# Kernel optimization log

Hardware: AMD Instinct MI355X
Metric: run time of the kernel (lower is better)

Reference implementation:

```python
import jax, jax.numpy as jnp
import numpy as np
import math

B, L, HID, H = 16, 1024, 1024, 16
E = HID // H
HALF = L // 2 + 1                      # 513 rfft bins
GLOBAL_RATIO = 0.6
LEFT = int(HALF * (1.0 - GLOBAL_RATIO))  # 205 (i=0, filter_mixer='G')
RIGHT = HALF                            # 513
FACTOR = 1
TOP_K = int(FACTOR * math.log(L))       # 6
LN_EPS = 1e-12


def setup_inputs() -> dict:
    key = jax.random.key(0)
    ks = jax.random.split(key, 12)
    s = 0.02
    return {
        "input_tensor": jax.random.normal(ks[0], (B, L, HID), jnp.float32),
        "attention_mask": jnp.zeros((B, 1, 1, L), jnp.float32),
        "Wq": jax.random.normal(ks[1], (HID, HID), jnp.float32) * s,
        "bq": jnp.zeros((HID,), jnp.float32),
        "Wk": jax.random.normal(ks[2], (HID, HID), jnp.float32) * s,
        "bk": jnp.zeros((HID,), jnp.float32),
        "Wv": jax.random.normal(ks[3], (HID, HID), jnp.float32) * s,
        "bv": jnp.zeros((HID,), jnp.float32),
        "Wd": jax.random.normal(ks[4], (HID, HID), jnp.float32) * s,
        "bd": jnp.zeros((HID,), jnp.float32),
        "gamma": jnp.ones((HID,), jnp.float32),
        "beta": jnp.zeros((HID,), jnp.float32),
    }


def _heads(x):  # [B,L,HID] -> [B,H,E,L]
    return x.reshape(B, L, H, E).transpose(0, 2, 3, 1)


def _layer_norm(x, gamma, beta):
    mu = jnp.mean(x, axis=-1, keepdims=True)
    var = jnp.var(x, axis=-1, keepdims=True)
    return (x - mu) / jnp.sqrt(var + LN_EPS) * gamma + beta


def reference(input_tensor, attention_mask, Wq, bq, Wk, bk, Wv, bv, Wd, bd, gamma, beta):
    # QKV projections -> [B,H,E,L]
    q = _heads(input_tensor @ Wq + bq)
    k = _heads(input_tensor @ Wk + bk)
    v = _heads(input_tensor @ Wv + bv)

    # FFT-based autocorrelation restricted to retained frequency band [LEFT,RIGHT)
    q_fft = jnp.fft.rfft(q, axis=-1)            # [B,H,E,HALF] complex64
    k_fft = jnp.fft.rfft(k, axis=-1)
    res = q_fft[..., LEFT:RIGHT] * jnp.conj(k_fft[..., LEFT:RIGHT])
    box = jnp.zeros((B, H, E, HALF), res.dtype).at[..., LEFT:RIGHT].set(res)
    corr = jnp.fft.irfft(box, n=L, axis=-1)     # [B,H,E,L]

    # time_delay_agg_training: topk shared delays, softmax-weighted roll aggregation
    mean_value = jnp.mean(corr, axis=(1, 2))            # [B,L]
    _, idx = jax.lax.top_k(jnp.mean(mean_value, axis=0), TOP_K)  # [TOP_K]
    weights = mean_value[:, idx]                         # [B,TOP_K]
    tmp_corr = jax.nn.softmax(weights, axis=-1)
    delays_agg = jnp.zeros_like(v)
    for i in range(TOP_K):  # TOP_K=6, fixed small loop
        pattern = jnp.roll(v, -idx[i], axis=-1)
        delays_agg = delays_agg + pattern * tmp_corr[:, i][:, None, None, None]

    # [B,H,E,L] -> [B,L,HID]
    context = delays_agg.transpose(0, 3, 1, 2).reshape(B, L, HID)
    hidden = context @ Wd + bd
    return _layer_norm(hidden + input_tensor, gamma, beta)
```

## Files before the change

kernel.cpp:

```cpp
#include <hip/hip_runtime.h>


typedef unsigned short u16;
typedef unsigned int   u32;
typedef __attribute__((ext_vector_type(8))) __bf16 bf16x8;
typedef __attribute__((ext_vector_type(4))) float  floatx4;

#define HIDn 1024

__device__ __forceinline__ u16 f2b(float f){ u32 i = __float_as_uint(f); return (u16)((i + 0x7fffu + ((i>>16)&1u)) >> 16); }

__device__ __forceinline__ void gl_lds16(const u16* g, u16* l){
  __builtin_amdgcn_global_load_lds((__attribute__((address_space(1))) const void*)g,
                                   (__attribute__((address_space(3))) void*)l, 16, 0, 0);
}

__device__ __forceinline__ void bar(){
  asm volatile("" ::: "memory");
  __builtin_amdgcn_s_barrier();
  asm volatile("" ::: "memory");
}
__device__ __forceinline__ void lgkm0(){
  asm volatile("s_waitcnt lgkmcnt(0)" ::: "memory");
  __builtin_amdgcn_sched_barrier(0);
}

__global__ void fill_kernel(float* __restrict__ out, float v, int n)
{
  const int i = blockIdx.x*blockDim.x + threadIdx.x;
  if (i < n) out[i] = v;
}

__global__ __launch_bounds__(1024)
void prep_kernel(const float* __restrict__ x, u16* __restrict__ xb,
                 float* __restrict__ cbuf, int* __restrict__ ctrs,
                 const float* __restrict__ Wq, const float* __restrict__ Wk,
                 const float* __restrict__ Wv, const float* __restrict__ Wd,
                 u16* __restrict__ WqkvT, u16* __restrict__ WdT)
{
  __shared__ float tile[32][33];
  if (blockIdx.x < 2048){
    const int i = blockIdx.x*1024 + threadIdx.x;
    if (i < 16384) cbuf[i] = 0.f;
    if (blockIdx.x == 0 && threadIdx.x < 8) ctrs[threadIdx.x] = 0;
    const float4* xp = (const float4*)x;
    const float4 a = xp[2*i], b = xp[2*i+1];
    uint4 o;
    o.x = (u32)f2b(a.x) | ((u32)f2b(a.y)<<16);
    o.y = (u32)f2b(a.z) | ((u32)f2b(a.w)<<16);
    o.z = (u32)f2b(b.x) | ((u32)f2b(b.y)<<16);
    o.w = (u32)f2b(b.z) | ((u32)f2b(b.w)<<16);
    ((uint4*)xb)[i] = o;
  } else {
    const int bb  = blockIdx.x - 2048;
    const int mat = bb >> 10;
    const int rem = bb & 1023;
    const int bxT = rem & 31, byT = rem >> 5;
    const int tx = threadIdx.x & 31, ty = threadIdx.x >> 5;
    const float* W = (mat==0)?Wq:(mat==1)?Wk:(mat==2)?Wv:Wd;
    const int k = byT*32 + ty, n = bxT*32 + tx;
    tile[ty][tx] = W[(long)k*HIDn + n];
    __syncthreads();
    const int on = bxT*32 + ty, ok = byT*32 + tx;
    const u16 val = f2b(tile[tx][ty]);
    if (mat < 3) WqkvT[(long)(mat*HIDn + on)*HIDn + ok] = val;
    else         WdT[(long)on*HIDn + ok] = val;
  }
}

template<int EPI>
__global__ __launch_bounds__(512, 2)
void gemm_mfma(const u16* __restrict__ A, int lda, long sA,
               const u16* __restrict__ Bt, int ldb, long sB,
               void* __restrict__ C0, u16* __restrict__ o1, u16* __restrict__ o2,
               int ldc, int K,
               const float* __restrict__ b0, const float* __restrict__ b1,
               const float* __restrict__ b2, const float* __restrict__ resid,
               float* __restrict__ cbuf, int* __restrict__ ctrs,
               const float* __restrict__ gam, const float* __restrict__ bet,
               int* __restrict__ idxo, float* __restrict__ wo)
{
  __shared__ __align__(16) u16 As[2][16384];
  __shared__ __align__(16) u16 Bs[2][16384];
  __shared__ float bins[512];
  __shared__ int lastf;

  const int gx = gridDim.x, gy = gridDim.y;
  const int lin = (blockIdx.z*gy + blockIdx.y)*gx + blockIdx.x;
  const int cpx = (gx*gy*gridDim.z) >> 3;
  const int swz = (lin & 7)*cpx + (lin >> 3);
  const int bx  = swz % gx;
  const int byz = swz / gx;
  const int by  = byz % gy;
  const int bz  = byz / gy;

  const int tid  = threadIdx.x;
  const int wave = tid >> 6, lane = tid & 63;
  const int waveM = wave >> 2, waveN = wave & 3;
  const int qd = lane >> 4, ln = lane & 15, rl = ln & 7;
  const u16* Ab = A  + (long)bz * sA;
  const u16* Bb = Bt + (long)bz * sB;
  const int aRow0 = by * 256, bRow0 = bx * 256;
  const int nt = K >> 6;

  const int s0 = wave*128 + lane;
  const int r0 = s0 >> 3, r1 = r0 + 8;
  const int kc = ((s0 & 7) ^ (r0 & 7)) * 8;
  const long aOff0 = (long)(aRow0 + r0)*lda + kc;
  const long aOff1 = (long)(aRow0 + r1)*lda + kc;
  const long bOff0 = (long)(bRow0 + r0)*ldb + kc;
  const long bOff1 = (long)(bRow0 + r1)*ldb + kc;
  const int dstW = wave*1024;

#define STAGE_A(p, h, kt) do{ \
    gl_lds16(Ab + aOff0 + (long)(h)*128*lda + (kt), &As[p][(h)*8192 + dstW]); \
    gl_lds16(Ab + aOff1 + (long)(h)*128*lda + (kt), &As[p][(h)*8192 + dstW + 512]); }while(0)
#define STAGE_B(p, h, kt) do{ \
    gl_lds16(Bb + bOff0 + (long)(h)*128*ldb + (kt), &Bs[p][(h)*8192 + dstW]); \
    gl_lds16(Bb + bOff1 + (long)(h)*128*ldb + (kt), &Bs[p][(h)*8192 + dstW + 512]); }while(0)

  if (EPI == 3) bins[tid] = 0.f;

  floatx4 acc[8][4];
  const floatx4 z4 = {0.f, 0.f, 0.f, 0.f};
  #pragma unroll
  for (int i=0;i<8;++i)
    #pragma unroll
    for (int j=0;j<4;++j) acc[i][j] = z4;

  const int aRd = (waveM*128 + ln)*64;
  const int bRd = (waveN*64  + ln)*64;
  const int csw0 = ((0 + qd) ^ rl) * 8;
  const int csw1 = ((4 + qd) ^ rl) * 8;

  bf16x8 av0[4], av1[4];
  bf16x8 bvA0[2], bvA1[2];
  bf16x8 bvB0[2], bvB1[2];

#define DS_AV(BUF, MH) do{ const u16* Ap_ = &As[BUF][0]; \
    _Pragma("unroll") for (int mi=0;mi<4;++mi){ \
      av0[mi] = *(const bf16x8*)(Ap_ + aRd + (MH)*4096 + mi*1024 + csw0); \
      av1[mi] = *(const bf16x8*)(Ap_ + aRd + (MH)*4096 + mi*1024 + csw1); } }while(0)
#define DS_BV(BUF, NH, d0_, d1_) do{ const u16* Bp_ = &Bs[BUF][0]; \
    _Pragma("unroll") for (int ni=0;ni<2;++ni){ \
      d0_[ni] = *(const bf16x8*)(Bp_ + bRd + ((NH)*2+ni)*1024 + csw0); \
      d1_[ni] = *(const bf16x8*)(Bp_ + bRd + ((NH)*2+ni)*1024 + csw1); } }while(0)
#define MFMAQ(MH, NH, b0_, b1_) do{ \
    __builtin_amdgcn_sched_barrier(0); \
    __builtin_amdgcn_s_setprio(1); \
    _Pragma("unroll") for (int mi=0;mi<4;++mi) \
      _Pragma("unroll") for (int ni=0;ni<2;++ni){ \
        acc[(MH)*4+mi][(NH)*2+ni] = __builtin_amdgcn_mfma_f32_16x16x32_bf16(av0[mi], b0_[ni], acc[(MH)*4+mi][(NH)*2+ni],0,0,0); \
        acc[(MH)*4+mi][(NH)*2+ni] = __builtin_amdgcn_mfma_f32_16x16x32_bf16(av1[mi], b1_[ni], acc[(MH)*4+mi][(NH)*2+ni],0,0,0); } \
    __builtin_amdgcn_s_setprio(0); \
    __builtin_amdgcn_sched_barrier(0); }while(0)

  STAGE_B(0,0,0);  STAGE_B(0,1,0);  STAGE_A(0,0,0);  STAGE_A(0,1,0);
  STAGE_B(1,0,64); STAGE_B(1,1,64); STAGE_A(1,0,64); STAGE_A(1,1,64);
  asm volatile("s_waitcnt vmcnt(8)" ::: "memory");
  bar();

  const int nIt = nt >> 1;
  for (int it = 0; it < nIt-1; ++it){
    const int k2 = (it*2+2) << 6;
    const int k3 = (it*2+3) << 6;
    DS_AV(0,0); DS_BV(0,0,bvA0,bvA1);
    bar(); lgkm0(); MFMAQ(0,0,bvA0,bvA1); bar();
    DS_BV(0,1,bvB0,bvB1);
    bar(); lgkm0(); MFMAQ(0,1,bvB0,bvB1); bar();
    DS_AV(0,1); STAGE_B(0,0,k2);
    bar(); lgkm0(); MFMAQ(1,0,bvA0,bvA1); bar();
    STAGE_B(0,1,k2);
    asm volatile("s_waitcnt vmcnt(4)" ::: "memory");
    bar(); MFMAQ(1,1,bvB0,bvB1); bar();
    DS_AV(1,0); DS_BV(1,0,bvA0,bvA1); STAGE_A(0,0,k2);
    bar(); lgkm0(); MFMAQ(0,0,bvA0,bvA1); bar();
    DS_BV(1,1,bvB0,bvB1); STAGE_A(0,1,k2);
    bar(); lgkm0(); MFMAQ(0,1,bvB0,bvB1); bar();
    DS_AV(1,1); STAGE_B(1,0,k3);
    bar(); lgkm0(); MFMAQ(1,0,bvA0,bvA1); bar();
    STAGE_B(1,1,k3); STAGE_A(1,0,k3); STAGE_A(1,1,k3);
    asm volatile("s_waitcnt vmcnt(8)" ::: "memory");
    bar(); MFMAQ(1,1,bvB0,bvB1); bar();
  }
  DS_AV(0,0); DS_BV(0,0,bvA0,bvA1);
  bar(); lgkm0(); MFMAQ(0,0,bvA0,bvA1); bar();
  DS_BV(0,1,bvB0,bvB1);
  bar(); lgkm0(); MFMAQ(0,1,bvB0,bvB1); bar();
  DS_AV(0,1);
  bar(); lgkm0(); MFMAQ(1,0,bvA0,bvA1); bar();
  asm volatile("s_waitcnt vmcnt(0)" ::: "memory");
  bar(); MFMAQ(1,1,bvB0,bvB1); bar();
  DS_AV(1,0); DS_BV(1,0,bvA0,bvA1);
  bar(); lgkm0(); MFMAQ(0,0,bvA0,bvA1); bar();
  DS_BV(1,1,bvB0,bvB1);
  bar(); lgkm0(); MFMAQ(0,1,bvB0,bvB1); bar();
  DS_AV(1,1);
  bar(); lgkm0(); MFMAQ(1,0,bvA0,bvA1); bar();
  MFMAQ(1,1,bvB0,bvB1);
#undef STAGE_A
#undef STAGE_B
#undef DS_AV
#undef DS_BV
#undef MFMAQ

  if (EPI == 3){
    float dsum[11][4];
    #pragma unroll
    for (int dd=0; dd<11; ++dd)
      #pragma unroll
      for (int r=0;r<4;++r) dsum[dd][r] = 0.f;
    #pragma unroll
    for (int mi=0;mi<8;++mi)
      #pragma unroll
      for (int ni=0;ni<4;++ni){
        const int dd = mi - ni + 3;
        #pragma unroll
        for (int r=0;r<4;++r) dsum[dd][r] += acc[mi][ni][r];
      }
    const int base = 255 + 128*waveM - 64*waveN + 4*qd - ln;
    #pragma unroll
    for (int dd=0; dd<11; ++dd)
      #pragma unroll
      for (int r=0;r<4;++r)
        atomicAdd(&bins[base + 16*(dd-3) + r], dsum[dd][r]);
    __syncthreads();
    if (tid < 511){
      const int d = (aRow0 - bRow0 + tid - 255) & 1023;
      atomicAdd(cbuf + bz*1024 + d, bins[tid]);
    }
    __syncthreads();
    if (tid == 0){
      __threadfence();
      const int nb = gx*gy*gridDim.z;
      lastf = (atomicAdd(ctrs, 1) == nb-1);
    }
    __syncthreads();
    if (!lastf) return;
    __threadfence();
    float* csh  = (float*)&As[0][0];
    float* gshp = (float*)&Bs[0][0];
    float* csum = gshp + 1024;
    float* vals = csum + 1024;
    float* wvp  = vals + 1024;
    int*   wip  = (int*)(wvp + 16);
    int*   chos = wip + 16;
    float* pw   = (float*)(chos + 8);
    for (int i = tid; i < 16384; i += 512) csh[i] = cbuf[i];
    __syncthreads();
    for (int l = tid; l < 1024; l += 512){
      float sc = 0.f;
      #pragma unroll
      for (int b = 0; b < 16; ++b) sc += csh[b*1024 + l];
      csum[l] = sc;
      float s;
      if (l == 0) s = 307.f;
      else {
        const float kk = 3.14159265358979e0f/1024.f;
        const int n1 = (307*l) & 2047, n2 = (716*l) & 2047;
        s = sinf((float)n1*kk) * cosf((float)n2*kk) / sinf((float)l*kk);
      }
      gshp[l] = (2.f*s + ((l & 1) ? -1.f : 1.f)) * (1.0f/1048576.0f);
    }
    __syncthreads();
    for (int l = tid; l < 1024; l += 512){
      float S = 0.f;
      #pragma unroll 4
      for (int m = 0; m < 1024; ++m) S += csum[m] * gshp[(l - m) & 1023];
      vals[l] = S;
    }
    __syncthreads();
    for (int r = 0; r < 6; ++r){
      float v1 = vals[tid], v2 = vals[tid + 512];
      float cv = v1; int ci = tid;
      if (v2 > v1){ cv = v2; ci = tid + 512; }
      #pragma unroll
      for (int off = 32; off > 0; off >>= 1){
        const float ov = __shfl_down(cv, off);
        const int   oi = __shfl_down(ci, off);
        if (ov > cv || (ov == cv && oi < ci)){ cv = ov; ci = oi; }
      }
      if (lane == 0){ wvp[wave] = cv; wip[wave] = ci; }
      __syncthreads();
      if (tid == 0){
        float bv = wvp[0]; int bi = wip[0];
        #pragma unroll
        for (int k2 = 1; k2 < 8; ++k2)
          if (wvp[k2] > bv || (wvp[k2] == bv && wip[k2] < bi)){ bv = wvp[k2]; bi = wip[k2]; }
        chos[r] = bi; idxo[r] = bi; vals[bi] = -3.0e38f;
      }
      __syncthreads();
    }
    if (tid < 384){
      const int p = tid >> 2, li = tid & 3;
      const int b = p / 6, i = p % 6, ch = chos[i];
      float a2 = 0.f;
      #pragma unroll 4
      for (int m = li*256; m < li*256 + 256; ++m) a2 += csh[b*1024 + m] * gshp[(ch - m) & 1023];
      a2 += __shfl_down(a2, 2);
      a2 += __shfl_down(a2, 1);
      if (li == 0) pw[p] = a2;
    }
    __syncthreads();
    if (tid < 16){
      float w[6]; float mx = -3.0e38f;
      #pragma unroll
      for (int i = 0; i < 6; ++i){ w[i] = pw[tid*6 + i]; mx = fmaxf(mx, w[i]); }
      float sum = 0.f;
      #pragma unroll
      for (int i = 0; i < 6; ++i){ w[i] = expf(w[i] - mx); sum += w[i]; }
      #pragma unroll
      for (int i = 0; i < 6; ++i) wo[tid*6 + i] = w[i] / sum;
    }
    return;
  }

  if (EPI == 0){
    const int which = bx >> 2;
    const float* bp = (which==0) ? b0 : ((which==1) ? b1 : b2);
    u16* Cb = (which==0) ? (u16*)C0 : ((which==1) ? o1 : o2);
    const int nb = bRow0 & 1023;
    #pragma unroll
    for (int mi=0;mi<8;++mi){
      const int gm = aRow0 + waveM*128 + mi*16 + qd*4;
      #pragma unroll
      for (int ni=0;ni<4;++ni){
        const int nl = nb + waveN*64 + ni*16 + ln;
        const float bias = bp[nl];
        #pragma unroll
        for (int r=0;r<4;++r) Cb[(long)(gm+r)*ldc + nl] = f2b(acc[mi][ni][r] + bias);
      }
    }
  } else {
    float* C = (float*)C0;
    #pragma unroll
    for (int mi=0;mi<8;++mi){
      const int gm = aRow0 + waveM*128 + mi*16 + qd*4;
      #pragma unroll
      for (int ni=0;ni<4;++ni){
        const int gn = bRow0 + waveN*64 + ni*16 + ln;
        const float bias = b0[gn];
        #pragma unroll
        for (int r=0;r<4;++r)
          C[(long)(gm+r)*ldc + gn] = acc[mi][ni][r] + bias + resid[(long)(gm+r)*ldc + gn];
      }
    }
    const int nb = gx*gy*gridDim.z;
    __syncthreads();
    if (tid == 0){
      __threadfence();
      atomicAdd(&ctrs[1], 1);
      while (atomicAdd(&ctrs[1], 0) < nb) __builtin_amdgcn_s_sleep(8);
    }
    __syncthreads();
    __threadfence();
    float* gsh_ = (float*)&As[0][0];
    float* bsh_ = gsh_ + 1024;
    for (int i = tid; i < 1024; i += 512){ gsh_[i] = gam[i]; bsh_[i] = bet[i]; }
    __syncthreads();
    const float4* g4 = (const float4*)gsh_;
    const float4* be4 = (const float4*)bsh_;
    const int row0 = lin*64 + wave*8;
    for (int rr = 0; rr < 8; ++rr){
      const int row = row0 + rr;
      float4* rp = (float4*)(C + (long)row*1024);
      float4 vv[4]; float s1 = 0.f, s2 = 0.f;
      #pragma unroll
      for (int j = 0; j < 4; ++j){
        vv[j] = rp[j*64 + lane];
        s1 += vv[j].x + vv[j].y + vv[j].z + vv[j].w;
        s2 += vv[j].x*vv[j].x + vv[j].y*vv[j].y + vv[j].z*vv[j].z + vv[j].w*vv[j].w;
      }
      #pragma unroll
      for (int off = 32; off > 0; off >>= 1){
        s1 += __shfl_xor(s1, off);
        s2 += __shfl_xor(s2, off);
      }
      const float mu   = s1 * (1.f/1024.f);
      const float var  = fmaxf(s2 * (1.f/1024.f) - mu*mu, 0.f);
      const float rstd = rsqrtf(var + 1e-12f);
      #pragma unroll
      for (int j = 0; j < 4; ++j){
        const int idx = j*64 + lane;
        const float4 g = g4[idx], be = be4[idx];
        float4 o;
        o.x = (vv[j].x - mu)*rstd*g.x + be.x;
        o.y = (vv[j].y - mu)*rstd*g.y + be.y;
        o.z = (vv[j].z - mu)*rstd*g.z + be.z;
        o.w = (vv[j].w - mu)*rstd*g.w + be.w;
        rp[idx] = o;
      }
    }
  }
}

__global__ __launch_bounds__(256)
void context_kernel(const u16* __restrict__ Vb, const int* __restrict__ idx,
                    const float* __restrict__ w, u16* __restrict__ CT)
{
  const int lin = blockIdx.x;
  const int xcd = lin & 7, j = lin >> 3;
  const int row = xcd*2048 + j*2 + (threadIdx.x >> 7);
  const int b = row >> 10, l = row & 1023;
  const int t = threadIdx.x & 127;
  float wl[6]; int id[6];
  #pragma unroll
  for (int i = 0; i < 6; ++i){ id[i] = idx[i]; wl[i] = w[b*6 + i]; }
  float acc[8] = {0,0,0,0,0,0,0,0};
  #pragma unroll
  for (int i = 0; i < 6; ++i){
    const long src = (long)b*1024 + ((l + id[i]) & 1023);
    const uint4 pk = *(const uint4*)(Vb + src*1024 + t*8);
    const float ww = wl[i];
    union{float f; u32 u;} cv;
    cv.u = pk.x<<16;          acc[0] += ww*cv.f;
    cv.u = pk.x & 0xffff0000u; acc[1] += ww*cv.f;
    cv.u = pk.y<<16;          acc[2] += ww*cv.f;
    cv.u = pk.y & 0xffff0000u; acc[3] += ww*cv.f;
    cv.u = pk.z<<16;          acc[4] += ww*cv.f;
    cv.u = pk.z & 0xffff0000u; acc[5] += ww*cv.f;
    cv.u = pk.w<<16;          acc[6] += ww*cv.f;
    cv.u = pk.w & 0xffff0000u; acc[7] += ww*cv.f;
  }
  uint4 o;
  o.x = (u32)f2b(acc[0]) | ((u32)f2b(acc[1])<<16);
  o.y = (u32)f2b(acc[2]) | ((u32)f2b(acc[3])<<16);
  o.z = (u32)f2b(acc[4]) | ((u32)f2b(acc[5])<<16);
  o.w = (u32)f2b(acc[6]) | ((u32)f2b(acc[7])<<16);
  *(uint4*)(CT + (long)row*1024 + t*8) = o;
}

extern "C" void kernel_launch(void* const* d_in, const int* in_sizes, int n_in,
                              void* d_out, int out_size, void* d_ws, size_t ws_size,
                              hipStream_t stream)
{
  (void)in_sizes; (void)n_in;
  const float* x     = (const float*)d_in[0];
  const float* Wq    = (const float*)d_in[2];
  const float* bq    = (const float*)d_in[3];
  const float* Wk    = (const float*)d_in[4];
  const float* bk    = (const float*)d_in[5];
  const float* Wv    = (const float*)d_in[6];
  const float* bv    = (const float*)d_in[7];
  const float* Wd    = (const float*)d_in[8];
  const float* bd    = (const float*)d_in[9];
  const float* gamma = (const float*)d_in[10];
  const float* beta  = (const float*)d_in[11];
  float* outp = (float*)d_out;

  const size_t NEED = 142741952UL;
  if (ws_size < NEED){
    const int n = out_size/2;
    fill_kernel<<<(n+255)/256, 256, 0, stream>>>(outp, (float)ws_size, n);
    return;
  }
  char* ws = (char*)d_ws;
  u16*  xb    = (u16*)(ws);
  u16*  Qb    = (u16*)(ws + 33554432L);
  u16*  Kb    = (u16*)(ws + 67108864L);
  u16*  Vb    = (u16*)(ws + 100663296L);
  u16*  WqkvT = (u16*)(ws + 134217728L);
  u16*  WdT   = (u16*)(ws + 140509184L);
  float* cbuf = (float*)(ws + 142606336L);
  int*   ctrs = (int*)  (ws + 142671872L);
  int*   idxb = (int*)  (ws + 142741504L);
  float* wsm  = (float*)(ws + 142741568L);
  u16*  CT    = Qb;

  prep_kernel<<<6144, 1024, 0, stream>>>(x, xb, cbuf, ctrs, Wq, Wk, Wv, Wd, WqkvT, WdT);

  gemm_mfma<0><<<dim3(12,64,1), 512, 0, stream>>>(
      xb, 1024, 0L, WqkvT, 1024, 0L, Qb, Kb, Vb, 1024, 1024,
      bq, bk, bv, nullptr, nullptr, nullptr, nullptr, nullptr, nullptr, nullptr);

  gemm_mfma<3><<<dim3(4,4,16), 512, 0, stream>>>(
      Qb, 1024, 1048576L, Kb, 1024, 1048576L, nullptr, nullptr, nullptr, 0, 1024,
      nullptr, nullptr, nullptr, nullptr, cbuf, ctrs, nullptr, nullptr, idxb, wsm);

  context_kernel<<<8192, 256, 0, stream>>>(Vb, idxb, wsm, CT);

  gemm_mfma<2><<<dim3(4,64,1), 512, 0, stream>>>(
      CT, 1024, 0L, WdT, 1024, 0L, outp, nullptr, nullptr, 1024, 1024,
      bd, nullptr, nullptr, x, nullptr, ctrs, gamma, beta, nullptr, nullptr);
}
```

Measured before the change: 522.3 us.

## Move last-block top-k filter into separate parallel filter and topk kernels

Removes the last-block-done tail from the correlation GEMM, where one 512-thread block ran the 1024x1024 circular convolution, top-k and softmax serially. It is replaced by an 8-block filter kernel that splits the convolution across 8192 threads, followed by a single-block top-k/softmax kernel with a padded shared layout. This drops the atomic counter and threadfence from the GEMM. The cost is two extra kernel launches and a reload of cbuf from global memory.

```diff
diff --git a/kernel.cpp b/kernel.cpp
--- a/kernel.cpp
+++ b/kernel.cpp
@@ -23,6 +23,17 @@
 __device__ __forceinline__ void lgkm0(){
   asm volatile("s_waitcnt lgkmcnt(0)" ::: "memory");
   __builtin_amdgcn_sched_barrier(0);
+}
+
+__device__ __forceinline__ float gf_val(int d){
+  float s;
+  if (d == 0) s = 307.f;
+  else {
+    const float k = 3.14159265358979e0f/1024.f;
+    const int n1 = (307*d) & 2047, n2 = (716*d) & 2047;
+    s = sinf((float)n1*k) * cosf((float)n2*k) / sinf((float)d*k);
+  }
+  return (2.f*s + ((d & 1) ? -1.f : 1.f)) * (1.0f/1048576.0f);
 }
 
 __global__ void fill_kernel(float* __restrict__ out, float v, int n)
@@ -77,13 +88,11 @@
                const float* __restrict__ b0, const float* __restrict__ b1,
                const float* __restrict__ b2, const float* __restrict__ resid,
                float* __restrict__ cbuf, int* __restrict__ ctrs,
-               const float* __restrict__ gam, const float* __restrict__ bet,
-               int* __restrict__ idxo, float* __restrict__ wo)
+               const float* __restrict__ gam, const float* __restrict__ bet)
 {
   __shared__ __align__(16) u16 As[2][16384];
   __shared__ __align__(16) u16 Bs[2][16384];
   __shared__ float bins[512];
-  __shared__ int lastf;
 
   const int gx = gridDim.x, gy = gridDim.y;
   const int lin = (blockIdx.z*gy + blockIdx.y)*gx + blockIdx.x;
@@ -229,89 +238,6 @@
       const int d = (aRow0 - bRow0 + tid - 255) & 1023;
       atomicAdd(cbuf + bz*1024 + d, bins[tid]);
     }
-    __syncthreads();
-    if (tid == 0){
-      __threadfence();
-      const int nb = gx*gy*gridDim.z;
-      lastf = (atomicAdd(ctrs, 1) == nb-1);
-    }
-    __syncthreads();
-    if (!lastf) return;
-    __threadfence();
-    float* csh  = (float*)&As[0][0];
-    float* gshp = (float*)&Bs[0][0];
-    float* csum = gshp + 1024;
-    float* vals = csum + 1024;
-    float* wvp  = vals + 1024;
-    int*   wip  = (int*)(wvp + 16);
-    int*   chos = wip + 16;
-    float* pw   = (float*)(chos + 8);
-    for (int i = tid; i < 16384; i += 512) csh[i] = cbuf[i];
-    __syncthreads();
-    for (int l = tid; l < 1024; l += 512){
-      float sc = 0.f;
-      #pragma unroll
-      for (int b = 0; b < 16; ++b) sc += csh[b*1024 + l];
-      csum[l] = sc;
-      float s;
-      if (l == 0) s = 307.f;
-      else {
-        const float kk = 3.14159265358979e0f/1024.f;
-        const int n1 = (307*l) & 2047, n2 = (716*l) & 2047;
-        s = sinf((float)n1*kk) * cosf((float)n2*kk) / sinf((float)l*kk);
-      }
-      gshp[l] = (2.f*s + ((l & 1) ? -1.f : 1.f)) * (1.0f/1048576.0f);
-    }
-    __syncthreads();
-    for (int l = tid; l < 1024; l += 512){
-      float S = 0.f;
-      #pragma unroll 4
-      for (int m = 0; m < 1024; ++m) S += csum[m] * gshp[(l - m) & 1023];
-      vals[l] = S;
-    }
-    __syncthreads();
-    for (int r = 0; r < 6; ++r){
-      float v1 = vals[tid], v2 = vals[tid + 512];
-      float cv = v1; int ci = tid;
-      if (v2 > v1){ cv = v2; ci = tid + 512; }
-      #pragma unroll
-      for (int off = 32; off > 0; off >>= 1){
-        const float ov = __shfl_down(cv, off);
-        const int   oi = __shfl_down(ci, off);
-        if (ov > cv || (ov == cv && oi < ci)){ cv = ov; ci = oi; }
-      }
-      if (lane == 0){ wvp[wave] = cv; wip[wave] = ci; }
-      __syncthreads();
-      if (tid == 0){
-        float bv = wvp[0]; int bi = wip[0];
-        #pragma unroll
-        for (int k2 = 1; k2 < 8; ++k2)
-          if (wvp[k2] > bv || (wvp[k2] == bv && wip[k2] < bi)){ bv = wvp[k2]; bi = wip[k2]; }
-        chos[r] = bi; idxo[r] = bi; vals[bi] = -3.0e38f;
-      }
-      __syncthreads();
-    }
-    if (tid < 384){
-      const int p = tid >> 2, li = tid & 3;
-      const int b = p / 6, i = p % 6, ch = chos[i];
-      float a2 = 0.f;
-      #pragma unroll 4
-      for (int m = li*256; m < li*256 + 256; ++m) a2 += csh[b*1024 + m] * gshp[(ch - m) & 1023];
-      a2 += __shfl_down(a2, 2);
-      a2 += __shfl_down(a2, 1);
-      if (li == 0) pw[p] = a2;
-    }
-    __syncthreads();
-    if (tid < 16){
-      float w[6]; float mx = -3.0e38f;
-      #pragma unroll
-      for (int i = 0; i < 6; ++i){ w[i] = pw[tid*6 + i]; mx = fmaxf(mx, w[i]); }
-      float sum = 0.f;
-      #pragma unroll
-      for (int i = 0; i < 6; ++i){ w[i] = expf(w[i] - mx); sum += w[i]; }
-      #pragma unroll
-      for (int i = 0; i < 6; ++i) wo[tid*6 + i] = w[i] / sum;
-    }
     return;
   }
 
@@ -391,6 +317,91 @@
         rp[idx] = o;
       }
     }
+  }
+}
+
+__global__ __launch_bounds__(1024)
+void filter_kernel(const float* __restrict__ c, float* __restrict__ S)
+{
+  __shared__ float csum[1024];
+  __shared__ float gsh[1024];
+  const int t = threadIdx.x;
+  float sc = 0.f;
+  #pragma unroll
+  for (int b = 0; b < 16; ++b) sc += c[b*1024 + t];
+  csum[t] = sc;
+  gsh[t] = gf_val(t);
+  __syncthreads();
+  const int l = blockIdx.x*128 + (t >> 3);
+  const int li = t & 7;
+  float a = 0.f;
+  #pragma unroll 8
+  for (int k = 0; k < 128; ++k){
+    const int m = li + 8*k;
+    a += csum[m] * gsh[(l - m) & 1023];
+  }
+  a += __shfl_down(a, 4); a += __shfl_down(a, 2); a += __shfl_down(a, 1);
+  if (li == 0) S[l] = a;
+}
+
+__global__ __launch_bounds__(1024)
+void topk_kernel(const float* __restrict__ c, const float* __restrict__ S,
+                 int* __restrict__ idxout, float* __restrict__ wout)
+{
+  __shared__ float csh[16*1025];
+  __shared__ float gsh[1024];
+  __shared__ float vals[1024];
+  __shared__ float wv[16];
+  __shared__ int   wi[16];
+  __shared__ int   chosen[6];
+  __shared__ float pw[96];
+  const int t = threadIdx.x, lane = t & 63, wid = t >> 6;
+  vals[t] = S[t];
+  gsh[t] = gf_val(t);
+  #pragma unroll
+  for (int b = 0; b < 16; ++b) csh[b*1025 + t] = c[b*1024 + t];
+  __syncthreads();
+  for (int r = 0; r < 6; ++r){
+    float cv = vals[t]; int ci = t;
+    #pragma unroll
+    for (int off = 32; off > 0; off >>= 1){
+      const float ov = __shfl_down(cv, off);
+      const int   oi = __shfl_down(ci, off);
+      if (ov > cv || (ov == cv && oi < ci)){ cv = ov; ci = oi; }
+    }
+    if (lane == 0){ wv[wid] = cv; wi[wid] = ci; }
+    __syncthreads();
+    if (t == 0){
+      float bv = wv[0]; int bi = wi[0];
+      #pragma unroll
+      for (int k = 1; k < 16; ++k)
+        if (wv[k] > bv || (wv[k] == bv && wi[k] < bi)){ bv = wv[k]; bi = wi[k]; }
+      chosen[r] = bi; idxout[r] = bi; vals[bi] = -3.0e38f;
+    }
+    __syncthreads();
+  }
+  if (t < 768){
+    const int p = t >> 3, li = t & 7;
+    const int b = p / 6, i = p - b*6, ch = chosen[i];
+    float a = 0.f;
+    #pragma unroll 8
+    for (int k = 0; k < 128; ++k){
+      const int m = li + 8*k;
+      a += csh[b*1025 + m] * gsh[(ch - m) & 1023];
+    }
+    a += __shfl_down(a, 4); a += __shfl_down(a, 2); a += __shfl_down(a, 1);
+    if (li == 0) pw[p] = a;
+  }
+  __syncthreads();
+  if (t < 16){
+    float w[6]; float mx = -3.0e38f;
+    #pragma unroll
+    for (int i = 0; i < 6; ++i){ w[i] = pw[t*6 + i]; mx = fmaxf(mx, w[i]); }
+    float sum = 0.f;
+    #pragma unroll
+    for (int i = 0; i < 6; ++i){ w[i] = expf(w[i] - mx); sum += w[i]; }
+    #pragma unroll
+    for (int i = 0; i < 6; ++i) wout[t*6 + i] = w[i] / sum;
   }
 }
 
@@ -462,7 +473,8 @@
   u16*  WqkvT = (u16*)(ws + 134217728L);
   u16*  WdT   = (u16*)(ws + 140509184L);
   float* cbuf = (float*)(ws + 142606336L);
-  int*   ctrs = (int*)  (ws + 142671872L);
+  float* sbuf = (float*)(ws + 142671872L);
+  int*   ctrs = (int*)  (ws + 142675968L);
   int*   idxb = (int*)  (ws + 142741504L);
   float* wsm  = (float*)(ws + 142741568L);
   u16*  CT    = Qb;
@@ -471,15 +483,17 @@
 
   gemm_mfma<0><<<dim3(12,64,1), 512, 0, stream>>>(
       xb, 1024, 0L, WqkvT, 1024, 0L, Qb, Kb, Vb, 1024, 1024,
-      bq, bk, bv, nullptr, nullptr, nullptr, nullptr, nullptr, nullptr, nullptr);
+      bq, bk, bv, nullptr, nullptr, nullptr, nullptr, nullptr);
 
   gemm_mfma<3><<<dim3(4,4,16), 512, 0, stream>>>(
       Qb, 1024, 1048576L, Kb, 1024, 1048576L, nullptr, nullptr, nullptr, 0, 1024,
-      nullptr, nullptr, nullptr, nullptr, cbuf, ctrs, nullptr, nullptr, idxb, wsm);
-
+      nullptr, nullptr, nullptr, nullptr, cbuf, nullptr, nullptr, nullptr);
+
+  filter_kernel<<<8, 1024, 0, stream>>>(cbuf, sbuf);
+  topk_kernel<<<1, 1024, 0, stream>>>(cbuf, sbuf, idxb, wsm);
   context_kernel<<<8192, 256, 0, stream>>>(Vb, idxb, wsm, CT);
 
   gemm_mfma<2><<<dim3(4,64,1), 512, 0, stream>>>(
       CT, 1024, 0L, WdT, 1024, 0L, outp, nullptr, nullptr, 1024, 1024,
-      bd, nullptr, nullptr, x, nullptr, ctrs, gamma, beta, nullptr, nullptr);
-}
+      bd, nullptr, nullptr, x, nullptr, ctrs, gamma, beta);
+}
```

After: 473.4 us. -9.4%, faster.
